# Kernel tuning notes

Hardware: AMD Instinct MI355X
Metric: run time of the kernel (lower is better)

## Reference

```python
import jax, jax.numpy as jnp
import numpy as np

BN_EPS = 1e-5
R = 8.0        # radius
L = 11         # sequence kernel size (odd), s = L//2
K = 24         # kernel_channels[-1]
N_NODES = 32768
N_EDGES = 524288
C_IN = 128     # in_channels == out_channels
C_W = 32       # width = out_channels * base_width / 64


def _bn(x, gamma, beta):
    # BatchNorm1d in training mode: biased batch statistics over node dim
    mu = jnp.mean(x, axis=0)
    var = jnp.mean(jnp.square(x - mu), axis=0)
    return (x - mu) * jax.lax.rsqrt(var + BN_EPS) * gamma + beta


def _lrelu(x, slope):
    return jnp.where(x >= 0, x, slope * x)


def setup_inputs() -> dict:
    key = jax.random.key(0)
    ks = jax.random.split(key, 10)

    def glorot(k, shape, fan_in):
        return jax.random.normal(k, shape, jnp.float32) * np.float32(1.0 / np.sqrt(fan_in))

    inp = {}
    inp["x"] = jax.random.normal(ks[0], (N_NODES, C_IN), jnp.float32)
    inp["pos"] = jax.random.normal(ks[1], (N_NODES, 3), jnp.float32) * 10.0
    inp["ori"] = jax.random.normal(ks[2], (N_NODES, 9), jnp.float32)
    inp["seq"] = jnp.arange(N_NODES, dtype=jnp.int32)
    inp["edge_index"] = jax.random.randint(ks[3], (2, N_EDGES), 0, N_NODES, jnp.int32)
    # input MLP params: BN(C_IN) -> LeakyReLU(0.1) -> Linear(C_IN->C_W, no bias) -> BN(C_W) -> LeakyReLU(0.1)
    inp["bn1_g"] = jnp.ones((C_IN,), jnp.float32)
    inp["bn1_b"] = jnp.zeros((C_IN,), jnp.float32)
    inp["lin1_w"] = glorot(ks[4], (C_IN, C_W), C_IN)
    inp["bn2_g"] = jnp.ones((C_W,), jnp.float32)
    inp["bn2_b"] = jnp.zeros((C_W,), jnp.float32)
    # CDConv WeightNet (single layer kernel_channels=[K]): per-seq-bin affine 7 -> K
    inp["wn_w"] = glorot(ks[5], (L, 7, K), 7)
    inp["wn_b"] = jnp.zeros((L, K), jnp.float32)
    # CDConv output projection: [K*C_W, C_W]
    inp["conv_w"] = glorot(ks[6], (K * C_W, C_W), K * C_W)
    # output Linear: BN(C_W) -> LeakyReLU(0.1) -> Linear(C_W->C_IN, no bias)
    inp["bn3_g"] = jnp.ones((C_W,), jnp.float32)
    inp["bn3_b"] = jnp.zeros((C_W,), jnp.float32)
    inp["lin2_w"] = glorot(ks[7], (C_W, C_IN), C_W)
    return inp


def reference(x, pos, ori, seq, edge_index,
              bn1_g, bn1_b, lin1_w, bn2_g, bn2_b,
              wn_w, wn_b, conv_w, bn3_g, bn3_b, lin2_w):
    n = x.shape[0]
    identity = x  # in_channels == out_channels -> identity branch is passthrough

    # ----- input MLP (mid_channels=None) -----
    h = _lrelu(_bn(x, bn1_g, bn1_b), 0.1)
    h = h @ lin1_w                       # [N, C_W]
    h = _lrelu(_bn(h, bn2_g, bn2_b), 0.1)

    # ----- CDConv: continuous geometric kernel over neighbor edges -----
    src, dst = edge_index[0], edge_index[1]      # message j=src -> i=dst
    d = pos[src] - pos[dst]                      # [E,3]
    dist = jnp.linalg.norm(d, axis=-1, keepdims=True)
    direction = d / (dist + 1e-9)
    Ri = ori[dst].reshape(-1, 3, 3)              # receiver local frame
    Rj = ori[src].reshape(-1, 3, 3)
    pos_local = jnp.einsum('eij,ej->ei', Ri, direction)      # direction in local frame
    ori_feat = jnp.einsum('eij,ej->ei', Ri, Rj[:, 0, :])     # neighbor axis in local frame
    delta = jnp.concatenate([pos_local, ori_feat, dist / R], axis=-1)  # [E,7]

    s = L // 2
    sidx = jnp.clip(seq[src] - seq[dst], -s, s) + s          # [E] in [0, L)

    # WeightNet: per-edge affine selected by sequence bin, LeakyReLU(0.2)
    w = _lrelu(jnp.einsum('ef,efk->ek', delta, wn_w[sidx]) + wn_b[sidx], 0.2)  # [E,K]

    # message = outer(kernel_weight, x_j), scatter-sum to receivers
    msg = (w[:, :, None] * h[src][:, None, :]).reshape(w.shape[0], K * C_W)   # [E, K*C_W]
    agg = jax.ops.segment_sum(msg, dst, num_segments=n)                        # [N, K*C_W]
    h = agg @ conv_w                                                            # [N, C_W]

    # ----- output Linear + residual -----
    h = _lrelu(_bn(h, bn3_g, bn3_b), 0.1)
    out = h @ lin2_w + identity
    return out
```

## Files before the change

### kernel.cpp

```cpp
#include <hip/hip_runtime.h>

#define N_NODES 32768
#define C_IN 128
#define C_W 32
#define KK 24
#define SS 5
#define GG 8
#define AGS (KK * C_W + 4)
#define TCAP 256

__global__ void __launch_bounds__(256) k_pre(
        const float* __restrict__ x, float* __restrict__ s1,
        const int* __restrict__ ei, int E, int* __restrict__ counts) {
    int t = threadIdx.x;
    int c = t % C_IN;
    int r0 = blockIdx.x * 2 + t / C_IN;
    float s = 0.f, sq = 0.f;
    for (int r = r0; r < N_NODES; r += 1024) {
        float v = x[(size_t)r * C_IN + c];
        s += v; sq += v * v;
    }
    atomicAdd(&s1[c], s);
    atomicAdd(&s1[C_IN + c], sq);
    for (int e = blockIdx.x * 256 + t; e < E; e += 512 * 256)
        atomicAdd(&counts[ei[E + e]], 1);
}

__global__ void __launch_bounds__(256) k_mlp1(
        const float* __restrict__ x, const float* __restrict__ s1,
        const float* __restrict__ g1, const float* __restrict__ b1,
        const float* __restrict__ w1, float* __restrict__ hpre,
        float* __restrict__ s2sh) {
    __shared__ float sAB[2][C_IN];
    __shared__ float sx[32][C_IN + 4];
    __shared__ float sw[C_IN][C_W];
    const int t = threadIdx.x;
    const int row0 = blockIdx.x * 32;
    if (t < C_IN) {
        float mean = s1[t] * (1.f / N_NODES);
        float var = s1[C_IN + t] * (1.f / N_NODES) - mean * mean;
        float a = g1[t] * rsqrtf(var + 1e-5f);
        sAB[0][t] = a; sAB[1][t] = b1[t] - mean * a;
    }
    for (int idx = t; idx < C_IN * C_W; idx += 256)
        sw[idx / C_W][idx % C_W] = w1[idx];
    __syncthreads();
    for (int idx = t; idx < 32 * 32; idx += 256) {
        int r = idx >> 5, cq = idx & 31;
        float4 v = *(const float4*)&x[(size_t)(row0 + r) * C_IN + cq * 4];
        float* d = &sx[r][cq * 4];
        float a0 = sAB[0][cq*4+0]*v.x + sAB[1][cq*4+0];
        float a1 = sAB[0][cq*4+1]*v.y + sAB[1][cq*4+1];
        float a2 = sAB[0][cq*4+2]*v.z + sAB[1][cq*4+2];
        float a3 = sAB[0][cq*4+3]*v.w + sAB[1][cq*4+3];
        d[0] = a0 >= 0.f ? a0 : 0.1f * a0;
        d[1] = a1 >= 0.f ? a1 : 0.1f * a1;
        d[2] = a2 >= 0.f ? a2 : 0.1f * a2;
        d[3] = a3 >= 0.f ? a3 : 0.1f * a3;
    }
    __syncthreads();
    const int r = t >> 3, c0 = (t & 7) * 4;
    float ac0 = 0.f, ac1 = 0.f, ac2 = 0.f, ac3 = 0.f;
    #pragma unroll 8
    for (int cc = 0; cc < C_IN; ++cc) {
        float xv = sx[r][cc];
        float4 wv = *(const float4*)&sw[cc][c0];
        ac0 += xv * wv.x; ac1 += xv * wv.y; ac2 += xv * wv.z; ac3 += xv * wv.w;
    }
    float4 o; o.x = ac0; o.y = ac1; o.z = ac2; o.w = ac3;
    *(float4*)&hpre[(size_t)(row0 + r) * C_W + c0] = o;
    __syncthreads();
    sx[r][c0] = ac0; sx[r][c0+1] = ac1; sx[r][c0+2] = ac2; sx[r][c0+3] = ac3;
    __syncthreads();
    if (t < C_W) {
        float s = 0.f, sq = 0.f;
        #pragma unroll
        for (int rr = 0; rr < 32; ++rr) {
            float v = sx[rr][t];
            s += v; sq += v * v;
        }
        int sh = (blockIdx.x & 7) * 64;
        atomicAdd(&s2sh[sh + t], s);
        atomicAdd(&s2sh[sh + C_W + t], sq);
    }
}

__global__ void __launch_bounds__(1024) k_scan(
        const int* __restrict__ counts, int* __restrict__ offsets,
        int* __restrict__ cursor) {
    __shared__ int sblk[1024];
    const int t = threadIdx.x;
    const int base = t * 32;
    const int4* cp = (const int4*)(counts + base);
    int loc[32];
    int s = 0;
    #pragma unroll
    for (int q = 0; q < 8; ++q) {
        int4 v = cp[q];
        loc[q*4+0] = s; s += v.x;
        loc[q*4+1] = s; s += v.y;
        loc[q*4+2] = s; s += v.z;
        loc[q*4+3] = s; s += v.w;
    }
    sblk[t] = s;
    __syncthreads();
    for (int d = 1; d < 1024; d <<= 1) {
        int u = (t >= d) ? sblk[t - d] : 0;
        __syncthreads();
        sblk[t] += u;
        __syncthreads();
    }
    const int blockbase = sblk[t] - s;
    #pragma unroll
    for (int q = 0; q < 8; ++q) {
        int4 o;
        o.x = blockbase + loc[q*4+0];
        o.y = blockbase + loc[q*4+1];
        o.z = blockbase + loc[q*4+2];
        o.w = blockbase + loc[q*4+3];
        ((int4*)(offsets + base))[q] = o;
        ((int4*)(cursor + base))[q] = o;
    }
    if (t == 1023) offsets[N_NODES] = sblk[1023];
}

__global__ void __launch_bounds__(256) k_edge(
        const int* __restrict__ ei, int E,
        const float* __restrict__ pos, const float* __restrict__ ori,
        const int* __restrict__ seq,
        const float* __restrict__ wnw, const float* __restrict__ wnb,
        int* __restrict__ cursor, int* __restrict__ srcPerm,
        unsigned int* __restrict__ wPerm) {
    __shared__ float sWnw[11][169];
    __shared__ float sWnb[11][24];
    const int t = threadIdx.x;
    for (int idx = t; idx < 11 * 168; idx += 256)
        sWnw[idx / 168][idx % 168] = wnw[idx];
    for (int idx = t; idx < 11 * 24; idx += 256)
        sWnb[idx / 24][idx % 24] = wnb[idx];
    __syncthreads();
    const int e = blockIdx.x * 256 + t;
    if (e >= E) return;
    const int src = ei[e];
    const int dst = ei[E + e];
    int ds = seq[src] - seq[dst];
    ds = ds < -SS ? -SS : (ds > SS ? SS : ds);
    const int sb = ds + SS;
    float dx = pos[src * 3 + 0] - pos[dst * 3 + 0];
    float dy = pos[src * 3 + 1] - pos[dst * 3 + 1];
    float dz = pos[src * 3 + 2] - pos[dst * 3 + 2];
    float dist = sqrtf(dx * dx + dy * dy + dz * dz);
    float inv = 1.f / (dist + 1e-9f);
    float ux = dx * inv, uy = dy * inv, uz = dz * inv;
    float b0 = ori[src * 9 + 0], b1 = ori[src * 9 + 1], b2 = ori[src * 9 + 2];
    float delta[7];
    #pragma unroll
    for (int r = 0; r < 3; ++r) {
        float m0 = ori[dst * 9 + r * 3 + 0];
        float m1 = ori[dst * 9 + r * 3 + 1];
        float m2 = ori[dst * 9 + r * 3 + 2];
        delta[r]     = m0 * ux + m1 * uy + m2 * uz;
        delta[3 + r] = m0 * b0 + m1 * b1 + m2 * b2;
    }
    delta[6] = dist * 0.125f;
    float w[KK];
    #pragma unroll
    for (int k = 0; k < KK; ++k) {
        float acc = sWnb[sb][k];
        #pragma unroll
        for (int f = 0; f < 7; ++f)
            acc += delta[f] * sWnw[sb][f * 24 + k];
        w[k] = acc >= 0.f ? acc : 0.2f * acc;
    }
    const int p = atomicAdd(&cursor[dst], 1);
    srcPerm[p] = src;
    unsigned int pk[12];
    #pragma unroll
    for (int jj = 0; jj < 12; ++jj) {
        unsigned int ulo = __float_as_uint(w[2*jj]);
        unsigned int uhi = __float_as_uint(w[2*jj+1]);
        ulo = (ulo + 0x7FFFu + ((ulo >> 16) & 1u)) >> 16;
        uhi = (uhi + 0x7FFFu + ((uhi >> 16) & 1u)) & 0xFFFF0000u;
        pk[jj] = uhi | ulo;
    }
    uint4* wp = (uint4*)(wPerm + (size_t)p * 12);
    uint4 o0; o0.x = pk[0]; o0.y = pk[1]; o0.z = pk[2]; o0.w = pk[3];
    uint4 o1; o1.x = pk[4]; o1.y = pk[5]; o1.z = pk[6]; o1.w = pk[7];
    uint4 o2; o2.x = pk[8]; o2.y = pk[9]; o2.z = pk[10]; o2.w = pk[11];
    wp[0] = o0; wp[1] = o1; wp[2] = o2;
}

#define BF_LO(u) __uint_as_float((u) << 16)
#define BF_HI(u) __uint_as_float((u) & 0xFFFF0000u)

__global__ void __launch_bounds__(512) k_node(
    const int* __restrict__ offsets, const int* __restrict__ srcPerm,
    const unsigned int* __restrict__ wPerm, const float* __restrict__ hpre,
    const float* __restrict__ s2sh, const float* __restrict__ g2,
    const float* __restrict__ b2, const float* __restrict__ convw,
    float* __restrict__ convout, float* __restrict__ s3sh) {

    __shared__ float sA2[C_W], sB2[C_W];
    __shared__ int sOff[GG + 1];
    __shared__ float sAgg[GG][AGS];
    __shared__ union SU {
        struct { unsigned int w[TCAP * 12]; int src[TCAP]; } stg;
        struct { float red[8][GG][C_W]; float rv[GG][C_W]; float rq[GG][C_W]; } fin;
    } U;

    const int t = threadIdx.x;
    const int i0 = blockIdx.x * GG;
    if (t < C_W) {
        float s = 0.f, sq = 0.f;
        #pragma unroll
        for (int j = 0; j < 8; ++j) {
            s  += s2sh[j * 64 + t];
            sq += s2sh[j * 64 + C_W + t];
        }
        float mean = s * (1.f / N_NODES);
        float var = sq * (1.f / N_NODES) - mean * mean;
        float a = g2[t] * rsqrtf(var + 1e-5f);
        sA2[t] = a; sB2[t] = b2[t] - mean * a;
    }
    if (t <= GG) sOff[t] = offsets[i0 + t];
    __syncthreads();

    const int w = t >> 6, lane = t & 63, c = lane & 31, s = lane >> 5;
    const float bnA = sA2[c], bnB = sB2[c];
    const int beg = sOff[w], end = sOff[w + 1];
    const int blkBeg = sOff[0], blkEnd = sOff[GG];
    float a[KK];
    #pragma unroll
    for (int k = 0; k < KK; ++k) a[k] = 0.f;

    for (int base = blkBeg; base < blkEnd; base += TCAP) {
        const int cnt = min(TCAP, blkEnd - base);
        __syncthreads();
        {
            const uint4* gw = (const uint4*)(wPerm + (size_t)base * 12);
            uint4* lw = (uint4*)U.stg.w;
            for (int u = t; u < cnt * 3; u += 512) lw[u] = gw[u];
            if (t < cnt) U.stg.src[t] = srcPerm[base + t];
        }
        __syncthreads();
        const int lo = max(beg, base) - base;
        const int hi = min(end, base + cnt) - base;
        for (int j8 = lo; j8 < hi; j8 += 8) {
            const int last = hi - 1;
            const int e0 = j8 + 0 + s, e1 = j8 + 2 + s;
            const int e2 = j8 + 4 + s, e3 = j8 + 6 + s;
            const int s0 = U.stg.src[min(e0, last)];
            const int s1 = U.stg.src[min(e1, last)];
            const int s2_ = U.stg.src[min(e2, last)];
            const int s3_ = U.stg.src[min(e3, last)];
            float h0 = hpre[(size_t)s0 * C_W + c];
            float h1 = hpre[(size_t)s1 * C_W + c];
            float h2 = hpre[(size_t)s2_ * C_W + c];
            float h3 = hpre[(size_t)s3_ * C_W + c];
            h0 = bnA*h0 + bnB; h0 = h0 >= 0.f ? h0 : 0.1f*h0; h0 = (e0 < hi) ? h0 : 0.f;
            h1 = bnA*h1 + bnB; h1 = h1 >= 0.f ? h1 : 0.1f*h1; h1 = (e1 < hi) ? h1 : 0.f;
            h2 = bnA*h2 + bnB; h2 = h2 >= 0.f ? h2 : 0.1f*h2; h2 = (e2 < hi) ? h2 : 0.f;
            h3 = bnA*h3 + bnB; h3 = h3 >= 0.f ? h3 : 0.1f*h3; h3 = (e3 < hi) ? h3 : 0.f;
            #pragma unroll
            for (int q = 0; q < 4; ++q) {
                const float v = q == 0 ? h0 : (q == 1 ? h1 : (q == 2 ? h2 : h3));
                const int ee = min(j8 + 2 * q + s, last);
                const uint4* wp = (const uint4*)&U.stg.w[ee * 12];
                const uint4 A = wp[0], B = wp[1], Cc = wp[2];
                a[0]  += BF_LO(A.x) * v;  a[1]  += BF_HI(A.x) * v;
                a[2]  += BF_LO(A.y) * v;  a[3]  += BF_HI(A.y) * v;
                a[4]  += BF_LO(A.z) * v;  a[5]  += BF_HI(A.z) * v;
                a[6]  += BF_LO(A.w) * v;  a[7]  += BF_HI(A.w) * v;
                a[8]  += BF_LO(B.x) * v;  a[9]  += BF_HI(B.x) * v;
                a[10] += BF_LO(B.y) * v;  a[11] += BF_HI(B.y) * v;
                a[12] += BF_LO(B.z) * v;  a[13] += BF_HI(B.z) * v;
                a[14] += BF_LO(B.w) * v;  a[15] += BF_HI(B.w) * v;
                a[16] += BF_LO(Cc.x) * v; a[17] += BF_HI(Cc.x) * v;
                a[18] += BF_LO(Cc.y) * v; a[19] += BF_HI(Cc.y) * v;
                a[20] += BF_LO(Cc.z) * v; a[21] += BF_HI(Cc.z) * v;
                a[22] += BF_LO(Cc.w) * v; a[23] += BF_HI(Cc.w) * v;
            }
        }
    }
    #pragma unroll
    for (int k = 0; k < KK; ++k) a[k] += __shfl_xor(a[k], 32, 64);
    if (s == 0) {
        #pragma unroll
        for (int k = 0; k < KK; ++k) sAgg[w][k * C_W + c] = a[k];
    }
    __syncthreads();

    {
        const int coq = t & 7;
        const int gp  = (t >> 3) & 7;
        const int sl8 = t >> 6;
        const int r0  = sl8 * 96;
        float4 acc; acc.x = acc.y = acc.z = acc.w = 0.f;
        #pragma unroll 6
        for (int rc = 0; rc < 96; rc += 4) {
            const float4 s4 = *(const float4*)&sAgg[gp][r0 + rc];
            const float4 w0 = *(const float4*)&convw[(size_t)(r0+rc+0)*32 + coq*4];
            const float4 w1 = *(const float4*)&convw[(size_t)(r0+rc+1)*32 + coq*4];
            const float4 w2 = *(const float4*)&convw[(size_t)(r0+rc+2)*32 + coq*4];
            const float4 w3 = *(const float4*)&convw[(size_t)(r0+rc+3)*32 + coq*4];
            acc.x += s4.x*w0.x + s4.y*w1.x + s4.z*w2.x + s4.w*w3.x;
            acc.y += s4.x*w0.y + s4.y*w1.y + s4.z*w2.y + s4.w*w3.y;
            acc.z += s4.x*w0.z + s4.y*w1.z + s4.z*w2.z + s4.w*w3.z;
            acc.w += s4.x*w0.w + s4.y*w1.w + s4.z*w2.w + s4.w*w3.w;
        }
        *(float4*)&U.fin.red[sl8][gp][coq * 4] = acc;
    }
    __syncthreads();
    if (t < 256) {
        const int gg = t >> 5, co = t & 31;
        float v = 0.f;
        #pragma unroll
        for (int sl = 0; sl < 8; ++sl) v += U.fin.red[sl][gg][co];
        convout[(size_t)(i0 + gg) * C_W + co] = v;
        U.fin.rv[gg][co] = v; U.fin.rq[gg][co] = v * v;
    }
    __syncthreads();
    if (t < 64) {
        int cc = t & 31;
        bool isq = t >= C_W;
        float s2 = 0.f;
        #pragma unroll
        for (int gg = 0; gg < GG; ++gg)
            s2 += isq ? U.fin.rq[gg][cc] : U.fin.rv[gg][cc];
        atomicAdd(&s3sh[(blockIdx.x & 7) * 64 + t], s2);
    }
}

__global__ void __launch_bounds__(256) k_out(
        const float* __restrict__ conv, const float* __restrict__ s3sh,
        const float* __restrict__ g3, const float* __restrict__ b3,
        const float* __restrict__ w2, const float* __restrict__ x,
        float* __restrict__ out) {
    __shared__ float sAB[2][C_W];
    __shared__ float sh[8][C_W];
    __shared__ float sw2[C_W][C_IN];
    const int t = threadIdx.x;
    const int row0 = blockIdx.x * 8;
    if (t < C_W) {
        float s = 0.f, sq = 0.f;
        #pragma unroll
        for (int j = 0; j < 8; ++j) {
            s  += s3sh[j * 64 + t];
            sq += s3sh[j * 64 + C_W + t];
        }
        float mean = s * (1.f / N_NODES);
        float var = sq * (1.f / N_NODES) - mean * mean;
        float a = g3[t] * rsqrtf(var + 1e-5f);
        sAB[0][t] = a; sAB[1][t] = b3[t] - mean * a;
    }
    for (int idx = t; idx < C_W * C_IN; idx += 256)
        sw2[idx >> 7][idx & 127] = w2[idx];
    __syncthreads();
    {
        float v = conv[(size_t)row0 * C_W + t];
        int r = t >> 5, cc = t & 31;
        v = sAB[0][cc] * v + sAB[1][cc];
        sh[r][cc] = v >= 0.f ? v : 0.1f * v;
    }
    __syncthreads();
    const int r = t >> 5, c4 = (t & 31) * 4;
    float4 acc = *(const float4*)&x[(size_t)(row0 + r) * C_IN + c4];
    #pragma unroll 8
    for (int cw = 0; cw < C_W; ++cw) {
        float hv = sh[r][cw];
        float4 wv = *(const float4*)&sw2[cw][c4];
        acc.x += hv * wv.x; acc.y += hv * wv.y;
        acc.z += hv * wv.z; acc.w += hv * wv.w;
    }
    *(float4*)&out[(size_t)(row0 + r) * C_IN + c4] = acc;
}

extern "C" void kernel_launch(void* const* d_in, const int* in_sizes, int n_in,
                              void* d_out, int out_size, void* d_ws, size_t ws_size,
                              hipStream_t stream) {
    const float* x     = (const float*)d_in[0];
    const float* pos   = (const float*)d_in[1];
    const float* ori   = (const float*)d_in[2];
    const int*   seq   = (const int*)d_in[3];
    const int*   ei    = (const int*)d_in[4];
    const float* bn1g  = (const float*)d_in[5];
    const float* bn1b  = (const float*)d_in[6];
    const float* lin1w = (const float*)d_in[7];
    const float* bn2g  = (const float*)d_in[8];
    const float* bn2b  = (const float*)d_in[9];
    const float* wnw   = (const float*)d_in[10];
    const float* wnb   = (const float*)d_in[11];
    const float* convw = (const float*)d_in[12];
    const float* bn3g  = (const float*)d_in[13];
    const float* bn3b  = (const float*)d_in[14];
    const float* lin2w = (const float*)d_in[15];
    float* out = (float*)d_out;
    const int E = in_sizes[4] / 2;

    char* wsb = (char*)d_ws;
    size_t off = 0;
    auto alloc = [&](size_t bytes) {
        void* p = wsb + off;
        off = (off + bytes + 255) & ~(size_t)255;
        return p;
    };
    float* s1      = (float*)alloc(256 * 4);
    float* s2sh    = (float*)alloc(512 * 4);
    float* s3sh    = (float*)alloc(512 * 4);
    int*   counts  = (int*)alloc((size_t)N_NODES * 4);
    size_t zero_bytes = off;
    int*   offsets = (int*)alloc(((size_t)N_NODES + 1) * 4);
    int*   cursor  = (int*)alloc((size_t)N_NODES * 4);
    int*   srcPerm = (int*)alloc((size_t)E * 4);
    float* hpre    = (float*)alloc((size_t)N_NODES * C_W * 4);
    float* convo   = (float*)alloc((size_t)N_NODES * C_W * 4);
    unsigned int* wPerm = (unsigned int*)alloc((size_t)E * 12 * 4);

    hipMemsetAsync(wsb, 0, zero_bytes, stream);

    k_pre<<<512, 256, 0, stream>>>(x, s1, ei, E, counts);
    k_scan<<<1, 1024, 0, stream>>>(counts, offsets, cursor);
    k_edge<<<(E + 255) / 256, 256, 0, stream>>>(ei, E, pos, ori, seq, wnw, wnb,
                                                cursor, srcPerm, wPerm);
    k_mlp1<<<N_NODES / 32, 256, 0, stream>>>(x, s1, bn1g, bn1b, lin1w, hpre, s2sh);
    k_node<<<N_NODES / GG, 512, 0, stream>>>(offsets, srcPerm, wPerm, hpre,
                                             s2sh, bn2g, bn2b, convw, convo, s3sh);
    k_out<<<N_NODES / 8, 256, 0, stream>>>(convo, s3sh, bn3g, bn3b, lin2w, x, out);
}
```

Before: 310.2 us.

## Pre-gather normalized bf16 source features into edge-sorted buffer in edge kernel

The MLP1 kernel now runs before the edge kernel. The edge kernel applies BN2 and LeakyReLU to each edge's source features and writes them as bf16 into a destination-sorted per-edge buffer. The node kernel then streams contiguous per-wave chunks of weights and features, with no srcPerm indirection, no random gather and no block-wide syncs. The cost is a larger scatter write from the edge kernel (64 extra bytes per edge) and an extra bf16 rounding on the features.

```diff
diff --git a/kernel.cpp b/kernel.cpp
--- a/kernel.cpp
+++ b/kernel.cpp
@@ -7,7 +7,9 @@
 #define SS 5
 #define GG 8
 #define AGS (KK * C_W + 4)
-#define TCAP 256
+
+#define BF_LO(u) __uint_as_float((u) << 16)
+#define BF_HI(u) __uint_as_float((u) & 0xFFFF0000u)
 
 __global__ void __launch_bounds__(256) k_pre(
         const float* __restrict__ x, float* __restrict__ s1,
@@ -129,15 +131,30 @@
         const float* __restrict__ pos, const float* __restrict__ ori,
         const int* __restrict__ seq,
         const float* __restrict__ wnw, const float* __restrict__ wnb,
-        int* __restrict__ cursor, int* __restrict__ srcPerm,
-        unsigned int* __restrict__ wPerm) {
+        const float* __restrict__ s2sh, const float* __restrict__ g2,
+        const float* __restrict__ b2, const float* __restrict__ hpre,
+        int* __restrict__ cursor,
+        unsigned int* __restrict__ wPerm, unsigned short* __restrict__ hPerm) {
     __shared__ float sWnw[11][169];
     __shared__ float sWnb[11][24];
+    __shared__ float sA2[C_W], sB2[C_W];
     const int t = threadIdx.x;
     for (int idx = t; idx < 11 * 168; idx += 256)
         sWnw[idx / 168][idx % 168] = wnw[idx];
     for (int idx = t; idx < 11 * 24; idx += 256)
         sWnb[idx / 24][idx % 24] = wnb[idx];
+    if (t < C_W) {
+        float s = 0.f, sq = 0.f;
+        #pragma unroll
+        for (int j = 0; j < 8; ++j) {
+            s  += s2sh[j * 64 + t];
+            sq += s2sh[j * 64 + C_W + t];
+        }
+        float mean = s * (1.f / N_NODES);
+        float var = sq * (1.f / N_NODES) - mean * mean;
+        float a = g2[t] * rsqrtf(var + 1e-5f);
+        sA2[t] = a; sB2[t] = b2[t] - mean * a;
+    }
     __syncthreads();
     const int e = blockIdx.x * 256 + t;
     if (e >= E) return;
@@ -152,7 +169,7 @@
     float dist = sqrtf(dx * dx + dy * dy + dz * dz);
     float inv = 1.f / (dist + 1e-9f);
     float ux = dx * inv, uy = dy * inv, uz = dz * inv;
-    float b0 = ori[src * 9 + 0], b1 = ori[src * 9 + 1], b2 = ori[src * 9 + 2];
+    float b0 = ori[src * 9 + 0], b1 = ori[src * 9 + 1], b2v = ori[src * 9 + 2];
     float delta[7];
     #pragma unroll
     for (int r = 0; r < 3; ++r) {
@@ -160,7 +177,7 @@
         float m1 = ori[dst * 9 + r * 3 + 1];
         float m2 = ori[dst * 9 + r * 3 + 2];
         delta[r]     = m0 * ux + m1 * uy + m2 * uz;
-        delta[3 + r] = m0 * b0 + m1 * b1 + m2 * b2;
+        delta[3 + r] = m0 * b0 + m1 * b1 + m2 * b2v;
     }
     delta[6] = dist * 0.125f;
     float w[KK];
@@ -173,7 +190,6 @@
         w[k] = acc >= 0.f ? acc : 0.2f * acc;
     }
     const int p = atomicAdd(&cursor[dst], 1);
-    srcPerm[p] = src;
     unsigned int pk[12];
     #pragma unroll
     for (int jj = 0; jj < 12; ++jj) {
@@ -183,103 +199,98 @@
         uhi = (uhi + 0x7FFFu + ((uhi >> 16) & 1u)) & 0xFFFF0000u;
         pk[jj] = uhi | ulo;
     }
-    uint4* wp = (uint4*)(wPerm + (size_t)p * 12);
-    uint4 o0; o0.x = pk[0]; o0.y = pk[1]; o0.z = pk[2]; o0.w = pk[3];
-    uint4 o1; o1.x = pk[4]; o1.y = pk[5]; o1.z = pk[6]; o1.w = pk[7];
-    uint4 o2; o2.x = pk[8]; o2.y = pk[9]; o2.z = pk[10]; o2.w = pk[11];
-    wp[0] = o0; wp[1] = o1; wp[2] = o2;
-}
-
-#define BF_LO(u) __uint_as_float((u) << 16)
-#define BF_HI(u) __uint_as_float((u) & 0xFFFF0000u)
+    {
+        uint4* wp = (uint4*)(wPerm + (size_t)p * 12);
+        uint4 o0; o0.x = pk[0]; o0.y = pk[1]; o0.z = pk[2]; o0.w = pk[3];
+        uint4 o1; o1.x = pk[4]; o1.y = pk[5]; o1.z = pk[6]; o1.w = pk[7];
+        uint4 o2; o2.x = pk[8]; o2.y = pk[9]; o2.z = pk[10]; o2.w = pk[11];
+        wp[0] = o0; wp[1] = o1; wp[2] = o2;
+    }
+    {
+        uint4* hp = (uint4*)(hPerm + (size_t)p * C_W);
+        const float4* hs = (const float4*)(hpre + (size_t)src * C_W);
+        #pragma unroll
+        for (int g = 0; g < 4; ++g) {
+            float4 v0 = hs[2*g], v1 = hs[2*g+1];
+            float f[8];
+            f[0]=v0.x; f[1]=v0.y; f[2]=v0.z; f[3]=v0.w;
+            f[4]=v1.x; f[5]=v1.y; f[6]=v1.z; f[7]=v1.w;
+            unsigned int o[4];
+            #pragma unroll
+            for (int j = 0; j < 4; ++j) {
+                int cc = g * 8 + 2 * j * 1;
+                float a0 = sA2[g*8+2*j]   * f[2*j]   + sB2[g*8+2*j];
+                float a1 = sA2[g*8+2*j+1] * f[2*j+1] + sB2[g*8+2*j+1];
+                a0 = a0 >= 0.f ? a0 : 0.1f * a0;
+                a1 = a1 >= 0.f ? a1 : 0.1f * a1;
+                unsigned int ulo = __float_as_uint(a0);
+                unsigned int uhi = __float_as_uint(a1);
+                ulo = (ulo + 0x7FFFu + ((ulo >> 16) & 1u)) >> 16;
+                uhi = (uhi + 0x7FFFu + ((uhi >> 16) & 1u)) & 0xFFFF0000u;
+                o[j] = uhi | ulo;
+                (void)cc;
+            }
+            uint4 ov; ov.x = o[0]; ov.y = o[1]; ov.z = o[2]; ov.w = o[3];
+            hp[g] = ov;
+        }
+    }
+}
 
 __global__ void __launch_bounds__(512) k_node(
-    const int* __restrict__ offsets, const int* __restrict__ srcPerm,
-    const unsigned int* __restrict__ wPerm, const float* __restrict__ hpre,
-    const float* __restrict__ s2sh, const float* __restrict__ g2,
-    const float* __restrict__ b2, const float* __restrict__ convw,
+    const int* __restrict__ offsets,
+    const unsigned int* __restrict__ wPerm, const unsigned short* __restrict__ hPerm,
+    const float* __restrict__ convw,
     float* __restrict__ convout, float* __restrict__ s3sh) {
 
-    __shared__ float sA2[C_W], sB2[C_W];
     __shared__ int sOff[GG + 1];
     __shared__ float sAgg[GG][AGS];
     __shared__ union SU {
-        struct { unsigned int w[TCAP * 12]; int src[TCAP]; } stg;
+        unsigned int w[GG][16 * 12];
         struct { float red[8][GG][C_W]; float rv[GG][C_W]; float rq[GG][C_W]; } fin;
     } U;
 
     const int t = threadIdx.x;
     const int i0 = blockIdx.x * GG;
-    if (t < C_W) {
-        float s = 0.f, sq = 0.f;
-        #pragma unroll
-        for (int j = 0; j < 8; ++j) {
-            s  += s2sh[j * 64 + t];
-            sq += s2sh[j * 64 + C_W + t];
-        }
-        float mean = s * (1.f / N_NODES);
-        float var = sq * (1.f / N_NODES) - mean * mean;
-        float a = g2[t] * rsqrtf(var + 1e-5f);
-        sA2[t] = a; sB2[t] = b2[t] - mean * a;
-    }
     if (t <= GG) sOff[t] = offsets[i0 + t];
     __syncthreads();
 
     const int w = t >> 6, lane = t & 63, c = lane & 31, s = lane >> 5;
-    const float bnA = sA2[c], bnB = sB2[c];
     const int beg = sOff[w], end = sOff[w + 1];
-    const int blkBeg = sOff[0], blkEnd = sOff[GG];
+    unsigned int* sWw = U.w[w];
     float a[KK];
     #pragma unroll
     for (int k = 0; k < KK; ++k) a[k] = 0.f;
 
-    for (int base = blkBeg; base < blkEnd; base += TCAP) {
-        const int cnt = min(TCAP, blkEnd - base);
-        __syncthreads();
-        {
-            const uint4* gw = (const uint4*)(wPerm + (size_t)base * 12);
-            uint4* lw = (uint4*)U.stg.w;
-            for (int u = t; u < cnt * 3; u += 512) lw[u] = gw[u];
-            if (t < cnt) U.stg.src[t] = srcPerm[base + t];
-        }
-        __syncthreads();
-        const int lo = max(beg, base) - base;
-        const int hi = min(end, base + cnt) - base;
-        for (int j8 = lo; j8 < hi; j8 += 8) {
-            const int last = hi - 1;
-            const int e0 = j8 + 0 + s, e1 = j8 + 2 + s;
-            const int e2 = j8 + 4 + s, e3 = j8 + 6 + s;
-            const int s0 = U.stg.src[min(e0, last)];
-            const int s1 = U.stg.src[min(e1, last)];
-            const int s2_ = U.stg.src[min(e2, last)];
-            const int s3_ = U.stg.src[min(e3, last)];
-            float h0 = hpre[(size_t)s0 * C_W + c];
-            float h1 = hpre[(size_t)s1 * C_W + c];
-            float h2 = hpre[(size_t)s2_ * C_W + c];
-            float h3 = hpre[(size_t)s3_ * C_W + c];
-            h0 = bnA*h0 + bnB; h0 = h0 >= 0.f ? h0 : 0.1f*h0; h0 = (e0 < hi) ? h0 : 0.f;
-            h1 = bnA*h1 + bnB; h1 = h1 >= 0.f ? h1 : 0.1f*h1; h1 = (e1 < hi) ? h1 : 0.f;
-            h2 = bnA*h2 + bnB; h2 = h2 >= 0.f ? h2 : 0.1f*h2; h2 = (e2 < hi) ? h2 : 0.f;
-            h3 = bnA*h3 + bnB; h3 = h3 >= 0.f ? h3 : 0.1f*h3; h3 = (e3 < hi) ? h3 : 0.f;
-            #pragma unroll
-            for (int q = 0; q < 4; ++q) {
-                const float v = q == 0 ? h0 : (q == 1 ? h1 : (q == 2 ? h2 : h3));
-                const int ee = min(j8 + 2 * q + s, last);
-                const uint4* wp = (const uint4*)&U.stg.w[ee * 12];
-                const uint4 A = wp[0], B = wp[1], Cc = wp[2];
-                a[0]  += BF_LO(A.x) * v;  a[1]  += BF_HI(A.x) * v;
-                a[2]  += BF_LO(A.y) * v;  a[3]  += BF_HI(A.y) * v;
-                a[4]  += BF_LO(A.z) * v;  a[5]  += BF_HI(A.z) * v;
-                a[6]  += BF_LO(A.w) * v;  a[7]  += BF_HI(A.w) * v;
-                a[8]  += BF_LO(B.x) * v;  a[9]  += BF_HI(B.x) * v;
-                a[10] += BF_LO(B.y) * v;  a[11] += BF_HI(B.y) * v;
-                a[12] += BF_LO(B.z) * v;  a[13] += BF_HI(B.z) * v;
-                a[14] += BF_LO(B.w) * v;  a[15] += BF_HI(B.w) * v;
-                a[16] += BF_LO(Cc.x) * v; a[17] += BF_HI(Cc.x) * v;
-                a[18] += BF_LO(Cc.y) * v; a[19] += BF_HI(Cc.y) * v;
-                a[20] += BF_LO(Cc.z) * v; a[21] += BF_HI(Cc.z) * v;
-                a[22] += BF_LO(Cc.w) * v; a[23] += BF_HI(Cc.w) * v;
-            }
+    for (int cb = beg; cb < end; cb += 16) {
+        const int m = min(16, end - cb);
+        const uint4* gw = (const uint4*)(wPerm + (size_t)cb * 12);
+        if (lane < m * 3) ((uint4*)sWw)[lane] = gw[lane];
+        float hr[8];
+        #pragma unroll
+        for (int q = 0; q < 8; ++q) {
+            int e = cb + 2 * q + s;
+            hr[q] = (e < end)
+                ? __uint_as_float(((unsigned int)hPerm[(size_t)e * C_W + c]) << 16)
+                : 0.f;
+        }
+        #pragma unroll
+        for (int q = 0; q < 8; ++q) {
+            const float v = hr[q];
+            const int ee = min(2 * q + s, m - 1);
+            const uint4* wp = (const uint4*)&sWw[ee * 12];
+            const uint4 A = wp[0], B = wp[1], Cc = wp[2];
+            a[0]  += BF_LO(A.x) * v;  a[1]  += BF_HI(A.x) * v;
+            a[2]  += BF_LO(A.y) * v;  a[3]  += BF_HI(A.y) * v;
+            a[4]  += BF_LO(A.z) * v;  a[5]  += BF_HI(A.z) * v;
+            a[6]  += BF_LO(A.w) * v;  a[7]  += BF_HI(A.w) * v;
+            a[8]  += BF_LO(B.x) * v;  a[9]  += BF_HI(B.x) * v;
+            a[10] += BF_LO(B.y) * v;  a[11] += BF_HI(B.y) * v;
+            a[12] += BF_LO(B.z) * v;  a[13] += BF_HI(B.z) * v;
+            a[14] += BF_LO(B.w) * v;  a[15] += BF_HI(B.w) * v;
+            a[16] += BF_LO(Cc.x) * v; a[17] += BF_HI(Cc.x) * v;
+            a[18] += BF_LO(Cc.y) * v; a[19] += BF_HI(Cc.y) * v;
+            a[20] += BF_LO(Cc.z) * v; a[21] += BF_HI(Cc.z) * v;
+            a[22] += BF_LO(Cc.w) * v; a[23] += BF_HI(Cc.w) * v;
         }
     }
     #pragma unroll
@@ -411,19 +422,20 @@
     size_t zero_bytes = off;
     int*   offsets = (int*)alloc(((size_t)N_NODES + 1) * 4);
     int*   cursor  = (int*)alloc((size_t)N_NODES * 4);
-    int*   srcPerm = (int*)alloc((size_t)E * 4);
     float* hpre    = (float*)alloc((size_t)N_NODES * C_W * 4);
     float* convo   = (float*)alloc((size_t)N_NODES * C_W * 4);
-    unsigned int* wPerm = (unsigned int*)alloc((size_t)E * 12 * 4);
+    unsigned int*   wPerm = (unsigned int*)alloc((size_t)E * 12 * 4);
+    unsigned short* hPerm = (unsigned short*)alloc((size_t)E * C_W * 2);
 
     hipMemsetAsync(wsb, 0, zero_bytes, stream);
 
     k_pre<<<512, 256, 0, stream>>>(x, s1, ei, E, counts);
     k_scan<<<1, 1024, 0, stream>>>(counts, offsets, cursor);
+    k_mlp1<<<N_NODES / 32, 256, 0, stream>>>(x, s1, bn1g, bn1b, lin1w, hpre, s2sh);
     k_edge<<<(E + 255) / 256, 256, 0, stream>>>(ei, E, pos, ori, seq, wnw, wnb,
-                                                cursor, srcPerm, wPerm);
-    k_mlp1<<<N_NODES / 32, 256, 0, stream>>>(x, s1, bn1g, bn1b, lin1w, hpre, s2sh);
-    k_node<<<N_NODES / GG, 512, 0, stream>>>(offsets, srcPerm, wPerm, hpre,
-                                             s2sh, bn2g, bn2b, convw, convo, s3sh);
+                                                s2sh, bn2g, bn2b, hpre, cursor,
+                                                wPerm, hPerm);
+    k_node<<<N_NODES / GG, 512, 0, stream>>>(offsets, wPerm, hPerm, convw,
+                                             convo, s3sh);
     k_out<<<N_NODES / 8, 256, 0, stream>>>(convo, s3sh, bn3g, bn3b, lin2w, x, out);
 }
```

Measured after the change: 365.7 us. 1.18x slower.

## Fuse edge weight computation into node aggregation kernel, drop wPerm buffer

Applied to the files above, without the earlier changes.

The per-edge WeightNet computation moves out of the separate edge kernel and into the node aggregation kernel. Each block handles 4 receivers and recomputes the edge features from gathered pos/ori/seq of the sources plus receiver data cached in shared memory. The activated source features are staged as bf16 in shared memory once per edge instead of being gathered per lane. This removes the global write and read of the 48-byte-per-edge weight buffer and the extra gather work, at the cost of a larger shared footprint per block, more blocks with less parallelism per block, and WeightNet compute done by only one thread per edge inside the fused kernel.

```diff
diff --git a/kernel.cpp b/kernel.cpp
--- a/kernel.cpp
+++ b/kernel.cpp
@@ -5,9 +5,23 @@
 #define C_W 32
 #define KK 24
 #define SS 5
-#define GG 8
+#define NPB 4
+#define TC 256
 #define AGS (KK * C_W + 4)
-#define TCAP 256
+#define WNS 172
+#define WBS 28
+#define HS 36
+
+#define BF_LO(u) __uint_as_float((u) << 16)
+#define BF_HI(u) __uint_as_float((u) & 0xFFFF0000u)
+
+__device__ __forceinline__ unsigned int bf16pair(float lo, float hi) {
+    unsigned int ulo = __float_as_uint(lo);
+    unsigned int uhi = __float_as_uint(hi);
+    ulo = (ulo + 0x7FFFu + ((ulo >> 16) & 1u)) >> 16;
+    uhi = (uhi + 0x7FFFu + ((uhi >> 16) & 1u)) & 0xFFFF0000u;
+    return uhi | ulo;
+}
 
 __global__ void __launch_bounds__(256) k_pre(
         const float* __restrict__ x, float* __restrict__ s1,
@@ -124,92 +138,44 @@
     if (t == 1023) offsets[N_NODES] = sblk[1023];
 }
 
-__global__ void __launch_bounds__(256) k_edge(
-        const int* __restrict__ ei, int E,
-        const float* __restrict__ pos, const float* __restrict__ ori,
-        const int* __restrict__ seq,
-        const float* __restrict__ wnw, const float* __restrict__ wnb,
-        int* __restrict__ cursor, int* __restrict__ srcPerm,
-        unsigned int* __restrict__ wPerm) {
-    __shared__ float sWnw[11][169];
-    __shared__ float sWnb[11][24];
+__global__ void __launch_bounds__(256) k_scatter(
+        const int* __restrict__ ei, int E, int* __restrict__ cursor,
+        int* __restrict__ srcPerm) {
+    int e = blockIdx.x * 256 + threadIdx.x;
+    if (e < E) {
+        int dst = ei[E + e];
+        int p = atomicAdd(&cursor[dst], 1);
+        srcPerm[p] = ei[e];
+    }
+}
+
+__global__ void __launch_bounds__(256) k_mega(
+    const int* __restrict__ offsets, const int* __restrict__ srcPerm,
+    const float* __restrict__ pos, const float* __restrict__ ori,
+    const int* __restrict__ seq, const float* __restrict__ hpre,
+    const float* __restrict__ s2sh, const float* __restrict__ g2,
+    const float* __restrict__ b2,
+    const float* __restrict__ wnw, const float* __restrict__ wnb,
+    const float* __restrict__ convw,
+    float* __restrict__ convout, float* __restrict__ s3sh) {
+
+    __shared__ float sWnw[11 * WNS];
+    __shared__ float sWnb[11 * WBS];
+    __shared__ float sA2[C_W], sB2[C_W];
+    __shared__ int   sOff[NPB + 1];
+    __shared__ float sNd[NPB][13];
+    __shared__ union SU {
+        struct { unsigned short h[TC * HS]; unsigned int w[TC * 12]; } stg;
+        struct { float agg[NPB][AGS]; float red[8][NPB][C_W];
+                 float rv[NPB][C_W]; float rq[NPB][C_W]; } fin;
+    } U;
+
     const int t = threadIdx.x;
+    const int i0 = blockIdx.x * NPB;
     for (int idx = t; idx < 11 * 168; idx += 256)
-        sWnw[idx / 168][idx % 168] = wnw[idx];
+        sWnw[(idx / 168) * WNS + idx % 168] = wnw[idx];
     for (int idx = t; idx < 11 * 24; idx += 256)
-        sWnb[idx / 24][idx % 24] = wnb[idx];
-    __syncthreads();
-    const int e = blockIdx.x * 256 + t;
-    if (e >= E) return;
-    const int src = ei[e];
-    const int dst = ei[E + e];
-    int ds = seq[src] - seq[dst];
-    ds = ds < -SS ? -SS : (ds > SS ? SS : ds);
-    const int sb = ds + SS;
-    float dx = pos[src * 3 + 0] - pos[dst * 3 + 0];
-    float dy = pos[src * 3 + 1] - pos[dst * 3 + 1];
-    float dz = pos[src * 3 + 2] - pos[dst * 3 + 2];
-    float dist = sqrtf(dx * dx + dy * dy + dz * dz);
-    float inv = 1.f / (dist + 1e-9f);
-    float ux = dx * inv, uy = dy * inv, uz = dz * inv;
-    float b0 = ori[src * 9 + 0], b1 = ori[src * 9 + 1], b2 = ori[src * 9 + 2];
-    float delta[7];
-    #pragma unroll
-    for (int r = 0; r < 3; ++r) {
-        float m0 = ori[dst * 9 + r * 3 + 0];
-        float m1 = ori[dst * 9 + r * 3 + 1];
-        float m2 = ori[dst * 9 + r * 3 + 2];
-        delta[r]     = m0 * ux + m1 * uy + m2 * uz;
-        delta[3 + r] = m0 * b0 + m1 * b1 + m2 * b2;
-    }
-    delta[6] = dist * 0.125f;
-    float w[KK];
-    #pragma unroll
-    for (int k = 0; k < KK; ++k) {
-        float acc = sWnb[sb][k];
-        #pragma unroll
-        for (int f = 0; f < 7; ++f)
-            acc += delta[f] * sWnw[sb][f * 24 + k];
-        w[k] = acc >= 0.f ? acc : 0.2f * acc;
-    }
-    const int p = atomicAdd(&cursor[dst], 1);
-    srcPerm[p] = src;
-    unsigned int pk[12];
-    #pragma unroll
-    for (int jj = 0; jj < 12; ++jj) {
-        unsigned int ulo = __float_as_uint(w[2*jj]);
-        unsigned int uhi = __float_as_uint(w[2*jj+1]);
-        ulo = (ulo + 0x7FFFu + ((ulo >> 16) & 1u)) >> 16;
-        uhi = (uhi + 0x7FFFu + ((uhi >> 16) & 1u)) & 0xFFFF0000u;
-        pk[jj] = uhi | ulo;
-    }
-    uint4* wp = (uint4*)(wPerm + (size_t)p * 12);
-    uint4 o0; o0.x = pk[0]; o0.y = pk[1]; o0.z = pk[2]; o0.w = pk[3];
-    uint4 o1; o1.x = pk[4]; o1.y = pk[5]; o1.z = pk[6]; o1.w = pk[7];
-    uint4 o2; o2.x = pk[8]; o2.y = pk[9]; o2.z = pk[10]; o2.w = pk[11];
-    wp[0] = o0; wp[1] = o1; wp[2] = o2;
-}
-
-#define BF_LO(u) __uint_as_float((u) << 16)
-#define BF_HI(u) __uint_as_float((u) & 0xFFFF0000u)
-
-__global__ void __launch_bounds__(512) k_node(
-    const int* __restrict__ offsets, const int* __restrict__ srcPerm,
-    const unsigned int* __restrict__ wPerm, const float* __restrict__ hpre,
-    const float* __restrict__ s2sh, const float* __restrict__ g2,
-    const float* __restrict__ b2, const float* __restrict__ convw,
-    float* __restrict__ convout, float* __restrict__ s3sh) {
-
-    __shared__ float sA2[C_W], sB2[C_W];
-    __shared__ int sOff[GG + 1];
-    __shared__ float sAgg[GG][AGS];
-    __shared__ union SU {
-        struct { unsigned int w[TCAP * 12]; int src[TCAP]; } stg;
-        struct { float red[8][GG][C_W]; float rv[GG][C_W]; float rq[GG][C_W]; } fin;
-    } U;
-
-    const int t = threadIdx.x;
-    const int i0 = blockIdx.x * GG;
+        sWnb[(idx / 24) * WBS + idx % 24] = wnb[idx];
     if (t < C_W) {
         float s = 0.f, sq = 0.f;
         #pragma unroll
@@ -222,83 +188,123 @@
         float a = g2[t] * rsqrtf(var + 1e-5f);
         sA2[t] = a; sB2[t] = b2[t] - mean * a;
     }
-    if (t <= GG) sOff[t] = offsets[i0 + t];
+    if (t <= NPB) sOff[t] = offsets[i0 + t];
+    if (t < NPB * 13) {
+        int n = t / 13, f = t % 13;
+        float v;
+        if (f < 3)       v = pos[(i0 + n) * 3 + f];
+        else if (f < 12) v = ori[(i0 + n) * 9 + (f - 3)];
+        else             v = __int_as_float(seq[i0 + n]);
+        sNd[n][f] = v;
+    }
     __syncthreads();
 
     const int w = t >> 6, lane = t & 63, c = lane & 31, s = lane >> 5;
-    const float bnA = sA2[c], bnB = sB2[c];
     const int beg = sOff[w], end = sOff[w + 1];
-    const int blkBeg = sOff[0], blkEnd = sOff[GG];
+    const int blkBeg = sOff[0], blkEnd = sOff[NPB];
     float a[KK];
     #pragma unroll
     for (int k = 0; k < KK; ++k) a[k] = 0.f;
 
-    for (int base = blkBeg; base < blkEnd; base += TCAP) {
-        const int cnt = min(TCAP, blkEnd - base);
+    for (int base = blkBeg; base < blkEnd; base += TC) {
+        const int cnt = min(TC, blkEnd - base);
         __syncthreads();
-        {
-            const uint4* gw = (const uint4*)(wPerm + (size_t)base * 12);
-            uint4* lw = (uint4*)U.stg.w;
-            for (int u = t; u < cnt * 3; u += 512) lw[u] = gw[u];
-            if (t < cnt) U.stg.src[t] = srcPerm[base + t];
+        if (t < cnt) {
+            const int slot = base + t;
+            const int g = (slot >= sOff[1]) + (slot >= sOff[2]) + (slot >= sOff[3]);
+            const int src = srcPerm[slot];
+            float px = pos[src*3+0], py = pos[src*3+1], pz = pos[src*3+2];
+            float o0 = ori[src*9+0], o1 = ori[src*9+1], o2 = ori[src*9+2];
+            int sqs = seq[src];
+            float dx = px - sNd[g][0], dy = py - sNd[g][1], dz = pz - sNd[g][2];
+            float dist = sqrtf(dx*dx + dy*dy + dz*dz);
+            float inv = 1.f / (dist + 1e-9f);
+            float ux = dx*inv, uy = dy*inv, uz = dz*inv;
+            float df[7];
+            #pragma unroll
+            for (int r = 0; r < 3; ++r) {
+                float m0 = sNd[g][3 + r*3 + 0];
+                float m1 = sNd[g][3 + r*3 + 1];
+                float m2 = sNd[g][3 + r*3 + 2];
+                df[r]     = m0*ux + m1*uy + m2*uz;
+                df[3 + r] = m0*o0 + m1*o1 + m2*o2;
+            }
+            df[6] = dist * 0.125f;
+            int dsq = sqs - __float_as_int(sNd[g][12]);
+            dsq = dsq < -SS ? -SS : (dsq > SS ? SS : dsq);
+            const int sb = dsq + SS;
+            float wv[KK];
+            #pragma unroll
+            for (int k = 0; k < KK; ++k) wv[k] = sWnb[sb * WBS + k];
+            #pragma unroll
+            for (int f = 0; f < 7; ++f) {
+                float d_ = df[f];
+                #pragma unroll
+                for (int k = 0; k < KK; ++k)
+                    wv[k] += d_ * sWnw[sb * WNS + f * 24 + k];
+            }
+            #pragma unroll
+            for (int k = 0; k < KK; ++k) wv[k] = wv[k] >= 0.f ? wv[k] : 0.2f * wv[k];
+            #pragma unroll
+            for (int jj = 0; jj < 12; ++jj)
+                U.stg.w[t * 12 + jj] = bf16pair(wv[2*jj], wv[2*jj+1]);
+            const float4* hs = (const float4*)(hpre + (size_t)src * C_W);
+            uint2* hd = (uint2*)&U.stg.h[t * HS];
+            #pragma unroll
+            for (int g4 = 0; g4 < 4; ++g4) {
+                float4 v0 = hs[2*g4], v1 = hs[2*g4+1];
+                float f[8] = {v0.x, v0.y, v0.z, v0.w, v1.x, v1.y, v1.z, v1.w};
+                #pragma unroll
+                for (int j = 0; j < 8; ++j) {
+                    int ch = g4 * 8 + j;
+                    float av = sA2[ch] * f[j] + sB2[ch];
+                    f[j] = av >= 0.f ? av : 0.1f * av;
+                }
+                uint2 p0; p0.x = bf16pair(f[0], f[1]); p0.y = bf16pair(f[2], f[3]);
+                uint2 p1; p1.x = bf16pair(f[4], f[5]); p1.y = bf16pair(f[6], f[7]);
+                hd[2*g4] = p0; hd[2*g4+1] = p1;
+            }
         }
         __syncthreads();
-        const int lo = max(beg, base) - base;
-        const int hi = min(end, base + cnt) - base;
-        for (int j8 = lo; j8 < hi; j8 += 8) {
-            const int last = hi - 1;
-            const int e0 = j8 + 0 + s, e1 = j8 + 2 + s;
-            const int e2 = j8 + 4 + s, e3 = j8 + 6 + s;
-            const int s0 = U.stg.src[min(e0, last)];
-            const int s1 = U.stg.src[min(e1, last)];
-            const int s2_ = U.stg.src[min(e2, last)];
-            const int s3_ = U.stg.src[min(e3, last)];
-            float h0 = hpre[(size_t)s0 * C_W + c];
-            float h1 = hpre[(size_t)s1 * C_W + c];
-            float h2 = hpre[(size_t)s2_ * C_W + c];
-            float h3 = hpre[(size_t)s3_ * C_W + c];
-            h0 = bnA*h0 + bnB; h0 = h0 >= 0.f ? h0 : 0.1f*h0; h0 = (e0 < hi) ? h0 : 0.f;
-            h1 = bnA*h1 + bnB; h1 = h1 >= 0.f ? h1 : 0.1f*h1; h1 = (e1 < hi) ? h1 : 0.f;
-            h2 = bnA*h2 + bnB; h2 = h2 >= 0.f ? h2 : 0.1f*h2; h2 = (e2 < hi) ? h2 : 0.f;
-            h3 = bnA*h3 + bnB; h3 = h3 >= 0.f ? h3 : 0.1f*h3; h3 = (e3 < hi) ? h3 : 0.f;
-            #pragma unroll
-            for (int q = 0; q < 4; ++q) {
-                const float v = q == 0 ? h0 : (q == 1 ? h1 : (q == 2 ? h2 : h3));
-                const int ee = min(j8 + 2 * q + s, last);
-                const uint4* wp = (const uint4*)&U.stg.w[ee * 12];
-                const uint4 A = wp[0], B = wp[1], Cc = wp[2];
-                a[0]  += BF_LO(A.x) * v;  a[1]  += BF_HI(A.x) * v;
-                a[2]  += BF_LO(A.y) * v;  a[3]  += BF_HI(A.y) * v;
-                a[4]  += BF_LO(A.z) * v;  a[5]  += BF_HI(A.z) * v;
-                a[6]  += BF_LO(A.w) * v;  a[7]  += BF_HI(A.w) * v;
-                a[8]  += BF_LO(B.x) * v;  a[9]  += BF_HI(B.x) * v;
-                a[10] += BF_LO(B.y) * v;  a[11] += BF_HI(B.y) * v;
-                a[12] += BF_LO(B.z) * v;  a[13] += BF_HI(B.z) * v;
-                a[14] += BF_LO(B.w) * v;  a[15] += BF_HI(B.w) * v;
-                a[16] += BF_LO(Cc.x) * v; a[17] += BF_HI(Cc.x) * v;
-                a[18] += BF_LO(Cc.y) * v; a[19] += BF_HI(Cc.y) * v;
-                a[20] += BF_LO(Cc.z) * v; a[21] += BF_HI(Cc.z) * v;
-                a[22] += BF_LO(Cc.w) * v; a[23] += BF_HI(Cc.w) * v;
-            }
-        }
-    }
+        const int lo = max(beg, base), hi = min(end, base + cnt);
+        #pragma unroll 2
+        for (int p = lo + s; p < hi; p += 2) {
+            const int pr = p - base;
+            const float v = BF_LO((unsigned int)U.stg.h[pr * HS + c]);
+            const uint4* wp = (const uint4*)&U.stg.w[pr * 12];
+            const uint4 A = wp[0], B = wp[1], Cc = wp[2];
+            a[0]  += BF_LO(A.x) * v;  a[1]  += BF_HI(A.x) * v;
+            a[2]  += BF_LO(A.y) * v;  a[3]  += BF_HI(A.y) * v;
+            a[4]  += BF_LO(A.z) * v;  a[5]  += BF_HI(A.z) * v;
+            a[6]  += BF_LO(A.w) * v;  a[7]  += BF_HI(A.w) * v;
+            a[8]  += BF_LO(B.x) * v;  a[9]  += BF_HI(B.x) * v;
+            a[10] += BF_LO(B.y) * v;  a[11] += BF_HI(B.y) * v;
+            a[12] += BF_LO(B.z) * v;  a[13] += BF_HI(B.z) * v;
+            a[14] += BF_LO(B.w) * v;  a[15] += BF_HI(B.w) * v;
+            a[16] += BF_LO(Cc.x) * v; a[17] += BF_HI(Cc.x) * v;
+            a[18] += BF_LO(Cc.y) * v; a[19] += BF_HI(Cc.y) * v;
+            a[20] += BF_LO(Cc.z) * v; a[21] += BF_HI(Cc.z) * v;
+            a[22] += BF_LO(Cc.w) * v; a[23] += BF_HI(Cc.w) * v;
+        }
+    }
+    __syncthreads();
     #pragma unroll
     for (int k = 0; k < KK; ++k) a[k] += __shfl_xor(a[k], 32, 64);
     if (s == 0) {
         #pragma unroll
-        for (int k = 0; k < KK; ++k) sAgg[w][k * C_W + c] = a[k];
+        for (int k = 0; k < KK; ++k) U.fin.agg[w][k * C_W + c] = a[k];
     }
     __syncthreads();
 
     {
         const int coq = t & 7;
-        const int gp  = (t >> 3) & 7;
-        const int sl8 = t >> 6;
-        const int r0  = sl8 * 96;
+        const int gp  = (t >> 3) & 3;
+        const int sl  = t >> 5;
+        const int r0  = sl * 96;
         float4 acc; acc.x = acc.y = acc.z = acc.w = 0.f;
         #pragma unroll 6
         for (int rc = 0; rc < 96; rc += 4) {
-            const float4 s4 = *(const float4*)&sAgg[gp][r0 + rc];
+            const float4 s4 = *(const float4*)&U.fin.agg[gp][r0 + rc];
             const float4 w0 = *(const float4*)&convw[(size_t)(r0+rc+0)*32 + coq*4];
             const float4 w1 = *(const float4*)&convw[(size_t)(r0+rc+1)*32 + coq*4];
             const float4 w2 = *(const float4*)&convw[(size_t)(r0+rc+2)*32 + coq*4];
@@ -308,10 +314,10 @@
             acc.z += s4.x*w0.z + s4.y*w1.z + s4.z*w2.z + s4.w*w3.z;
             acc.w += s4.x*w0.w + s4.y*w1.w + s4.z*w2.w + s4.w*w3.w;
         }
-        *(float4*)&U.fin.red[sl8][gp][coq * 4] = acc;
-    }
-    __syncthreads();
-    if (t < 256) {
+        *(float4*)&U.fin.red[sl][gp][coq * 4] = acc;
+    }
+    __syncthreads();
+    if (t < 128) {
         const int gg = t >> 5, co = t & 31;
         float v = 0.f;
         #pragma unroll
@@ -325,7 +331,7 @@
         bool isq = t >= C_W;
         float s2 = 0.f;
         #pragma unroll
-        for (int gg = 0; gg < GG; ++gg)
+        for (int gg = 0; gg < NPB; ++gg)
             s2 += isq ? U.fin.rq[gg][cc] : U.fin.rv[gg][cc];
         atomicAdd(&s3sh[(blockIdx.x & 7) * 64 + t], s2);
     }
@@ -414,16 +420,15 @@
     int*   srcPerm = (int*)alloc((size_t)E * 4);
     float* hpre    = (float*)alloc((size_t)N_NODES * C_W * 4);
     float* convo   = (float*)alloc((size_t)N_NODES * C_W * 4);
-    unsigned int* wPerm = (unsigned int*)alloc((size_t)E * 12 * 4);
 
     hipMemsetAsync(wsb, 0, zero_bytes, stream);
 
     k_pre<<<512, 256, 0, stream>>>(x, s1, ei, E, counts);
     k_scan<<<1, 1024, 0, stream>>>(counts, offsets, cursor);
-    k_edge<<<(E + 255) / 256, 256, 0, stream>>>(ei, E, pos, ori, seq, wnw, wnb,
-                                                cursor, srcPerm, wPerm);
+    k_scatter<<<(E + 255) / 256, 256, 0, stream>>>(ei, E, cursor, srcPerm);
     k_mlp1<<<N_NODES / 32, 256, 0, stream>>>(x, s1, bn1g, bn1b, lin1w, hpre, s2sh);
-    k_node<<<N_NODES / GG, 512, 0, stream>>>(offsets, srcPerm, wPerm, hpre,
-                                             s2sh, bn2g, bn2b, convw, convo, s3sh);
+    k_mega<<<N_NODES / NPB, 256, 0, stream>>>(offsets, srcPerm, pos, ori, seq,
+                                              hpre, s2sh, bn2g, bn2b, wnw, wnb,
+                                              convw, convo, s3sh);
     k_out<<<N_NODES / 8, 256, 0, stream>>>(convo, s3sh, bn3g, bn3b, lin2w, x, out);
 }
```

New measurement: 284.6 us. 8.2% less time.
